# Optimization experiments

Measured on AMD Instinct MI355X. Metric: run time of the kernel, lower is better.

## Reference

```python
import jax, jax.numpy as jnp
import numpy as np
import math

# ---- hyperparameters (from __init__) ----
S = 64.0
M = 0.45
EASY_MARGIN = False
ALPHA = 0.0
BETA = 0.0
EPS_OT = 0.1   # self.eps
NITER = 6      # self.niter
COS_M = math.cos(M)
SIN_M = math.sin(M)
TH = math.cos(math.pi - M)
MM = math.sin(math.pi - M) * M

# ---- shapes ----
B = 24
D_EMB = 512
N_CLASSES = 10000
C_CH = 256   # channels -> number of OT points per image
H = 14       # spatial -> point dim H*H = 196


def setup_inputs() -> dict:
    key = jax.random.key(0)
    k1, k2, k3, k4 = jax.random.split(key, 4)
    embeddings = jax.random.normal(k1, (B, D_EMB), dtype=jnp.float32)
    conv_features = jax.random.normal(k2, (B, C_CH, H, H), dtype=jnp.float32)
    label = jax.random.randint(k3, (B,), 0, 8)
    # nn.init.normal_(kernel, std=0.01)
    kernel = jax.random.normal(k4, (D_EMB, N_CLASSES), dtype=jnp.float32) * 0.01
    return {"embeddings": embeddings, "conv_features": conv_features,
            "kernel": kernel, "label": label, "epoch": 1}


def _cdist(x, y):
    # Euclidean pairwise distance via GEMM: x (n,d), y (m,d) -> (n,m)
    x2 = jnp.sum(x * x, axis=-1)[:, None]
    y2 = jnp.sum(y * y, axis=-1)[None, :]
    d2 = jnp.maximum(x2 + y2 - 2.0 * (x @ y.T), 0.0)
    return jnp.sqrt(d2 + 1e-12)


def _sinkhorn_dist(x, y):
    # Entropic OT distance <T, C> with uniform marginals, log-domain Sinkhorn.
    C = _cdist(x, y)                       # (n, m)
    n, m = C.shape
    log_mu = -jnp.log(jnp.float32(n))
    log_nu = -jnp.log(jnp.float32(m))
    f = jnp.zeros((n,), C.dtype)
    g = jnp.zeros((m,), C.dtype)
    for _ in range(NITER):  # fixed 6 iterations
        f = -EPS_OT * jax.nn.logsumexp((g[None, :] - C) / EPS_OT + log_nu, axis=1)
        g = -EPS_OT * jax.nn.logsumexp((f[:, None] - C) / EPS_OT + log_mu, axis=0)
    T = jnp.exp((f[:, None] + g[None, :] - C) / EPS_OT + log_mu + log_nu)
    return jnp.sum(T * C)


def reference(embeddings, conv_features, kernel, label, epoch):
    b = embeddings.shape[0]
    emb = embeddings / jnp.linalg.norm(embeddings, axis=1, keepdims=True)
    kn = kernel / jnp.linalg.norm(kernel, axis=0, keepdims=True)
    cos_theta = jnp.clip(emb @ kn, -1.0, 1.0)          # (B, n_classes)
    origin_cos = cos_theta

    rows = jnp.arange(b)
    tl = cos_theta[rows, label]                         # target logit (B,)
    sin_t = jnp.sqrt(jnp.maximum(1.0 - tl * tl, 0.0))
    ctm = tl * COS_M - sin_t * SIN_M
    if EASY_MARGIN:
        ftl = jnp.where(tl > 0.0, ctm, tl)
    else:
        ftl = jnp.where(tl > TH, ctm, tl - MM)
    cos_theta = cos_theta.at[rows, label].set(ftl)
    arcfaceloss = cos_theta * S

    # ---- triplet mining on embedding cosine similarities ----
    dists = emb @ emb.T                                 # (B, B) cosine sims
    eq = label[:, None] == label[None, :]               # (B, B) same-class mask
    # diff_low[a,p,n] = cos(a,n) - cos(a,p)
    diff = dists[:, None, :] - dists[:, :, None]        # (a, p, n)
    valid = eq[:, :, None] & (~eq)[:, None, :] & (diff > -ALPHA)
    n_cosine_pair = jnp.sum(valid)

    if epoch >= 0:
        feats = conv_features.reshape(b, conv_features.shape[1], -1)  # (B, C, H*H)
        # batched Sinkhorn distance for all (a,b) image pairs: (B, B)
        D = jax.vmap(lambda xa: jax.vmap(lambda xb: _sinkhorn_dist(xa, xb))(feats))(feats)
        dis = jnp.maximum(D[:, :, None] - D[:, None, :], -BETA)       # (a, p, n)
        hit = valid & (dis > 0.0)
        ot_pair = jnp.sum(hit)
        wass = jnp.sum(jnp.where(hit, dis, 0.0))
        wass_loss = jnp.where(wass > 0.0,
                              wass / jnp.maximum(ot_pair, 1).astype(wass.dtype),
                              jnp.zeros((), wass.dtype))
    else:
        ot_pair = jnp.zeros((), jnp.int32)
        wass_loss = jnp.zeros(())

    return (arcfaceloss, wass_loss, origin_cos * S, n_cosine_pair, ot_pair)
```

## Files before the change

kernel.cpp:

```cpp
#include <hip/hip_runtime.h>
#include <math.h>

#define B_SZ 24
#define D_EMBD 512
#define N_CLS 10000
#define CC 256
#define HH 196

#define NPAIR 276
#define NARC 40
#define NGRAM 36

#define S_SCALE 64.0f
#define COS_M 0.9004471023526769f
#define SIN_M 0.43496553411123023f
#define TH_C (-0.9004471023526769f)
#define MM_C 0.19573449035005357f
#define KSC 14.4269504088896f
#define C2E 0.0693147180559945f

typedef short bfrag8 __attribute__((ext_vector_type(8)));
typedef float facc4 __attribute__((ext_vector_type(4)));

#if __has_builtin(__builtin_amdgcn_exp2f)
#define EXP2F(x) __builtin_amdgcn_exp2f(x)
#else
#define EXP2F(x) exp2f(x)
#endif
#if __has_builtin(__builtin_amdgcn_logf)
#define LOG2F(x) __builtin_amdgcn_logf(x)
#else
#define LOG2F(x) __log2f(x)
#endif

__device__ inline unsigned short f2bf_rne(float x) {
    union { float f; unsigned u; } cv; cv.f = x;
    unsigned r = cv.u + 0x7FFFu + ((cv.u >> 16) & 1u);
    return (unsigned short)(r >> 16);
}
__device__ inline float bf2f(unsigned short h) {
    union { unsigned u; float f; } cv; cv.u = ((unsigned)h) << 16; return cv.f;
}

__global__ __launch_bounds__(1024) void k_fused(const float* __restrict__ emb,
        const float* __restrict__ conv, const float* __restrict__ kern,
        const int* __restrict__ label, float* __restrict__ dists,
        float* __restrict__ Dmat, float* __restrict__ out) {
    const int t = threadIdx.x;
    const int bid = blockIdx.x;

    __shared__ __align__(16) char smem[65536];

    if (bid >= NPAIR) {
        const int sb = bid - NPAIR;
        if (sb >= NARC) {
            const int gid = sb - NARC;
            int l = t & 63, w16 = t >> 6;
            if (gid == 0 && t < B_SZ) Dmat[t * B_SZ + t] = 0.f;
            int pid = gid * 16 + w16;
            if (pid >= B_SZ * B_SZ) return;
            int i = pid / B_SZ, j = pid - (pid / B_SZ) * B_SZ;
            float sij = 0.f, sii = 0.f, sjj = 0.f;
            #pragma unroll
            for (int u = 0; u < 8; ++u) {
                float vi = emb[i*D_EMBD + u*64 + l];
                float vj = emb[j*D_EMBD + u*64 + l];
                sij = fmaf(vi, vj, sij); sii = fmaf(vi, vi, sii); sjj = fmaf(vj, vj, sjj);
            }
            #pragma unroll
            for (int o = 1; o < 64; o <<= 1) {
                sij += __shfl_xor(sij, o, 64);
                sii += __shfl_xor(sii, o, 64);
                sjj += __shfl_xor(sjj, o, 64);
            }
            if (l == 0) dists[pid] = sij * rsqrtf(sii * sjj);
            return;
        }

        float* es = (float*)smem;
        float* inv_s = es + B_SZ * D_EMBD;
        int* lab_s = (int*)(inv_s + B_SZ);

        {
            const float4* s4 = (const float4*)emb;
            float4* d4 = (float4*)es;
            #pragma unroll
            for (int i = 0; i < 3; ++i) d4[i*1024 + t] = s4[i*1024 + t];
        }
        if (t < B_SZ) lab_s[t] = label[t];
        __syncthreads();
        {
            int l = t & 63, w = t >> 6;
            for (int r = w; r < B_SZ; r += 16) {
                float s = 0.f;
                #pragma unroll
                for (int u = 0; u < 8; ++u) { float v = es[r*D_EMBD + u*64 + l]; s = fmaf(v, v, s); }
                #pragma unroll
                for (int o = 1; o < 64; o <<= 1) s += __shfl_xor(s, o, 64);
                if (l == 0) inv_s[r] = rsqrtf(s);
            }
        }
        __syncthreads();

        const int cc = t >> 2, kc = t & 3;
        const int col = sb * 256 + cc;
        const int cL = col < N_CLS ? col : N_CLS - 1;
        float acc[B_SZ];
        #pragma unroll
        for (int r = 0; r < B_SZ; ++r) acc[r] = 0.f;
        float cn = 0.f;
        const int kb0 = kc << 7;
        for (int u = 0; u < 32; ++u) {
            const int um = (u + kc) & 31;
            const int kb = kb0 + (um << 2);
            float kv0 = kern[(kb+0)*N_CLS + cL];
            float kv1 = kern[(kb+1)*N_CLS + cL];
            float kv2 = kern[(kb+2)*N_CLS + cL];
            float kv3 = kern[(kb+3)*N_CLS + cL];
            cn = fmaf(kv0,kv0,cn); cn = fmaf(kv1,kv1,cn);
            cn = fmaf(kv2,kv2,cn); cn = fmaf(kv3,kv3,cn);
            #pragma unroll
            for (int r = 0; r < B_SZ; ++r) {
                const float4 e = *(const float4*)&es[r*D_EMBD + kb];
                acc[r] = fmaf(e.x, kv0, acc[r]);
                acc[r] = fmaf(e.y, kv1, acc[r]);
                acc[r] = fmaf(e.z, kv2, acc[r]);
                acc[r] = fmaf(e.w, kv3, acc[r]);
            }
        }
        cn += __shfl_xor(cn, 1, 64); cn += __shfl_xor(cn, 2, 64);
        #pragma unroll
        for (int r = 0; r < B_SZ; ++r) {
            acc[r] += __shfl_xor(acc[r], 1, 64);
            acc[r] += __shfl_xor(acc[r], 2, 64);
        }
        if (kc == 0 && col < N_CLS) {
            const float invk = rsqrtf(cn);
            #pragma unroll
            for (int r = 0; r < B_SZ; ++r) {
                float cosv = fminf(fmaxf(acc[r] * inv_s[r] * invk, -1.f), 1.f);
                float oc = cosv * S_SCALE;
                float af = oc;
                if (lab_s[r] == col) {
                    float tl = cosv;
                    float sint = sqrtf(fmaxf(1.f - tl*tl, 0.f));
                    float ctm = tl*COS_M - sint*SIN_M;
                    float ftl = (tl > TH_C) ? ctm : (tl - MM_C);
                    af = ftl * S_SCALE;
                }
                out[r*N_CLS + col] = af;
                out[240001 + r*N_CLS + col] = oc;
            }
        }
        return;
    }

    unsigned short* Ah = (unsigned short*)smem;
    unsigned short* Al = Ah + 8192;
    unsigned short* Bh = Al + 8192;
    unsigned short* Bl = Bh + 8192;
    float* rowred = (float*)smem;
    float* colred = rowred + 1024;
    float* rm_l   = colred + 1024;
    float* z_l    = rm_l + 256;
    float* g_l    = z_l + 256;
    float* q_l    = g_l + 256;
    float* p_l    = q_l + 256;
    float* na_s   = p_l + 256;
    float* nb_s   = na_s + 256;
    float* wredF  = nb_s + 256;
    float* wredG  = wredF + 4;
    float* wredD  = wredG + 4;
    float* gsh    = wredD + 16;

    const int w = t >> 6;
    const int wr = w >> 2, wc = w & 3;
    const int q = (t >> 4) & 3, c0 = t & 15;
    const int R0 = wr * 64, C0 = wc * 64;

    int rem = bid, a = 0;
    while (rem >= 23 - a) { rem -= 23 - a; ++a; }
    int b = a + 1 + rem;
    const float* xa = conv + a*CC*HH;
    const float* xb = conv + b*CC*HH;

    const int sn = t >> 2;
    const int sch = t & 3;

    facc4 acc[4][4];
    #pragma unroll
    for (int i = 0; i < 4; ++i)
        #pragma unroll
        for (int j = 0; j < 4; ++j) acc[i][j] = (facc4){0.f, 0.f, 0.f, 0.f};

    float pa = 0.f, pb = 0.f;

    for (int ks = 0; ks < 224; ks += 32) {
        __syncthreads();
        #pragma unroll
        for (int p = 0; p < 2; ++p) {
            int k0 = ks + sch*8;
            const float* src = (p ? xb : xa) + sn*HH + k0;
            float v[8];
            if (k0 + 8 <= HH) {
                const float4* s4 = (const float4*)src;
                float4 u0 = s4[0], u1 = s4[1];
                v[0]=u0.x; v[1]=u0.y; v[2]=u0.z; v[3]=u0.w;
                v[4]=u1.x; v[5]=u1.y; v[6]=u1.z; v[7]=u1.w;
            } else {
                #pragma unroll
                for (int j = 0; j < 8; ++j) v[j] = (k0 + j < HH) ? src[j] : 0.f;
            }
            float ps = 0.f;
            union { unsigned short s[8]; bfrag8 v8; } uh, ul;
            #pragma unroll
            for (int j = 0; j < 8; ++j) {
                ps = fmaf(v[j], v[j], ps);
                unsigned short hb = f2bf_rne(v[j]);
                uh.s[j] = hb;
                ul.s[j] = f2bf_rne(v[j] - bf2f(hb));
            }
            if (p) pb += ps; else pa += ps;
            unsigned short* dh = (p ? Bh : Ah) + sn*32 + sch*8;
            unsigned short* dl = (p ? Bl : Al) + sn*32 + sch*8;
            *(bfrag8*)dh = uh.v8;
            *(bfrag8*)dl = ul.v8;
        }
        __syncthreads();
        bfrag8 bh4[4], bl4[4];
        #pragma unroll
        for (int tj = 0; tj < 4; ++tj) {
            int col = C0 + tj*16 + c0;
            bh4[tj] = *(const bfrag8*)(Bh + col*32 + q*8);
            bl4[tj] = *(const bfrag8*)(Bl + col*32 + q*8);
        }
        #pragma unroll
        for (int ti = 0; ti < 4; ++ti) {
            int row = R0 + ti*16 + c0;
            bfrag8 ah = *(const bfrag8*)(Ah + row*32 + q*8);
            bfrag8 al = *(const bfrag8*)(Al + row*32 + q*8);
            #pragma unroll
            for (int tj = 0; tj < 4; ++tj) {
                acc[ti][tj] = __builtin_amdgcn_mfma_f32_16x16x32_bf16(ah, bh4[tj], acc[ti][tj], 0, 0, 0);
                acc[ti][tj] = __builtin_amdgcn_mfma_f32_16x16x32_bf16(ah, bl4[tj], acc[ti][tj], 0, 0, 0);
                acc[ti][tj] = __builtin_amdgcn_mfma_f32_16x16x32_bf16(al, bh4[tj], acc[ti][tj], 0, 0, 0);
            }
        }
    }
    __syncthreads();

    pa += __shfl_xor(pa, 1, 64); pa += __shfl_xor(pa, 2, 64);
    pb += __shfl_xor(pb, 1, 64); pb += __shfl_xor(pb, 2, 64);
    if (sch == 0) { na_s[sn] = pa; nb_s[sn] = pb; }
    if (t < 256) p_l[t] = 1.f;
    if (t < 4) { wredG[t] = 0.f; wredF[t] = 8.f; }
    if (t == 0) *gsh = 0.f;
    __syncthreads();

    facc4 E[4][4];
    {
        float nbv[4];
        #pragma unroll
        for (int tj = 0; tj < 4; ++tj) nbv[tj] = nb_s[C0 + tj*16 + c0];
        #pragma unroll
        for (int ti = 0; ti < 4; ++ti) {
            facc4 nav = *(const facc4*)&na_s[R0 + ti*16 + q*4];
            #pragma unroll
            for (int tj = 0; tj < 4; ++tj) {
                #pragma unroll
                for (int r = 0; r < 4; ++r) {
                    float d2 = fmaxf(nav[r] + nbv[tj] - 2.f*acc[ti][tj][r], 0.f);
                    E[ti][tj][r] = KSC * sqrtf(d2 + 1e-12f);
                }
            }
        }
    }

    const int istar = ((c0&1)<<3) | ((c0&2)<<1) | ((c0&4)>>1) | ((c0&8)>>3);
    const int rowstar = R0 + (istar>>2)*16 + q*4 + (istar&3);
    const int tjstar = ((q&1)<<1) | (q>>1);
    const int colstar = C0 + tjstar*16 + c0;

    {
        float v16[16];
        #pragma unroll
        for (int ti = 0; ti < 4; ++ti)
            #pragma unroll
            for (int r = 0; r < 4; ++r)
                v16[ti*4+r] = fminf(fminf(E[ti][0][r], E[ti][1][r]),
                                    fminf(E[ti][2][r], E[ti][3][r]));
        #pragma unroll
        for (int p = 0; p < 4; ++p) {
            const int m = 1 << p, hsz = 8 >> p;
            const bool hi = (c0 >> p) & 1;
            #pragma unroll
            for (int j = 0; j < hsz; ++j) {
                float mine = hi ? v16[j+hsz] : v16[j];
                float send = hi ? v16[j] : v16[j+hsz];
                v16[j] = fminf(mine, __shfl_xor(send, m, 64));
            }
        }
        rowred[wc*256 + rowstar] = v16[0];
    }
    __syncthreads();
    if (t < 256)
        rm_l[t] = fminf(fminf(rowred[t], rowred[256+t]), fminf(rowred[512+t], rowred[768+t]));
    __syncthreads();

    #pragma unroll
    for (int ti = 0; ti < 4; ++ti) {
        facc4 rmv = *(const facc4*)&rm_l[R0 + ti*16 + q*4];
        #pragma unroll
        for (int tj = 0; tj < 4; ++tj)
            #pragma unroll
            for (int r = 0; r < 4; ++r)
                E[ti][tj][r] = EXP2F(rmv[r] - E[ti][tj][r]);
    }

    #pragma unroll 1
    for (int it = 0; it < 6; ++it) {
        float Gstale = fmaxf(fmaxf(wredG[0], wredG[1]), fmaxf(wredG[2], wredG[3]));
        float MS     = fmaxf(fmaxf(wredF[0], wredF[1]), fmaxf(wredF[2], wredF[3]));
        float P4[4];
        #pragma unroll
        for (int tj = 0; tj < 4; ++tj) P4[tj] = p_l[C0 + tj*16 + c0];
        float v16[16];
        #pragma unroll
        for (int ti = 0; ti < 4; ++ti)
            #pragma unroll
            for (int r = 0; r < 4; ++r) {
                float s = 0.f;
                #pragma unroll
                for (int tj = 0; tj < 4; ++tj) s = fmaf(E[ti][tj][r], P4[tj], s);
                v16[ti*4+r] = s;
            }
        #pragma unroll
        for (int p = 0; p < 4; ++p) {
            const int m = 1 << p, hsz = 8 >> p;
            const bool hi = (c0 >> p) & 1;
            #pragma unroll
            for (int j = 0; j < hsz; ++j) {
                float mine = hi ? v16[j+hsz] : v16[j];
                float send = hi ? v16[j] : v16[j+hsz];
                v16[j] = mine + __shfl_xor(send, m, 64);
            }
        }
        rowred[wc*256 + rowstar] = v16[0];
        __syncthreads();
        if (t < 256) {
            float GS = *gsh;
            float s = rowred[t] + rowred[256+t] + rowred[512+t] + rowred[768+t];
            float z = 8.f - GS - LOG2F(s);
            z_l[t] = z;
            q_l[t] = EXP2F(z - MS);
            float m = z;
            #pragma unroll
            for (int o = 1; o < 64; o <<= 1) m = fmaxf(m, __shfl_xor(m, o, 64));
            if ((t & 63) == 0) wredF[t >> 6] = m;
        }
        __syncthreads();
        float Q[16];
        #pragma unroll
        for (int ti = 0; ti < 4; ++ti) {
            facc4 qv = *(const facc4*)&q_l[R0 + ti*16 + q*4];
            #pragma unroll
            for (int r = 0; r < 4; ++r) Q[ti*4+r] = qv[r];
        }
        float w4[4];
        #pragma unroll
        for (int tj = 0; tj < 4; ++tj) {
            float s = 0.f;
            #pragma unroll
            for (int ti = 0; ti < 4; ++ti)
                #pragma unroll
                for (int r = 0; r < 4; ++r) s = fmaf(E[ti][tj][r], Q[ti*4+r], s);
            w4[tj] = s;
        }
        #pragma unroll
        for (int p = 0; p < 2; ++p) {
            const int m = 16 << p, hsz = 2 >> p;
            const bool hi = (q >> p) & 1;
            #pragma unroll
            for (int j = 0; j < hsz; ++j) {
                float mine = hi ? w4[j+hsz] : w4[j];
                float send = hi ? w4[j] : w4[j+hsz];
                w4[j] = mine + __shfl_xor(send, m, 64);
            }
        }
        colred[wr*256 + colstar] = w4[0];
        __syncthreads();
        if (t < 256) {
            float s = colred[t] + colred[256+t] + colred[512+t] + colred[768+t];
            float G = 8.f - MS - LOG2F(s);
            g_l[t] = G;
            p_l[t] = EXP2F(G - Gstale);
            float m = G;
            #pragma unroll
            for (int o = 1; o < 64; o <<= 1) m = fmaxf(m, __shfl_xor(m, o, 64));
            if ((t & 63) == 0) wredG[t >> 6] = m;
            if (t == 0) *gsh = Gstale;
        }
        __syncthreads();
    }

    {
        float G4[4];
        #pragma unroll
        for (int tj = 0; tj < 4; ++tj) G4[tj] = g_l[C0 + tj*16 + c0] - 16.f;
        float d = 0.f;
        #pragma unroll
        for (int ti = 0; ti < 4; ++ti) {
            facc4 zv = *(const facc4*)&z_l[R0 + ti*16 + q*4];
            facc4 rmv = *(const facc4*)&rm_l[R0 + ti*16 + q*4];
            #pragma unroll
            for (int tj = 0; tj < 4; ++tj) {
                #pragma unroll
                for (int r = 0; r < 4; ++r) {
                    float e = fmaxf(E[ti][tj][r], 1e-45f);
                    float lE = LOG2F(e);
                    float ce = rmv[r] - lE;
                    d = fmaf(EXP2F(zv[r] + G4[tj] + lE), ce, d);
                }
            }
        }
        d *= C2E;
        #pragma unroll
        for (int o = 1; o < 64; o <<= 1) d += __shfl_xor(d, o, 64);
        if ((t & 63) == 0) wredD[w] = d;
        __syncthreads();
        if (t == 0) {
            float s = 0.f;
            #pragma unroll
            for (int i = 0; i < 16; ++i) s += wredD[i];
            Dmat[a*B_SZ + b] = s;
            Dmat[b*B_SZ + a] = s;
        }
    }
}

__global__ __launch_bounds__(256) void k_fin(const int* __restrict__ label,
        const float* __restrict__ dists, const float* __restrict__ Dmat,
        float* __restrict__ out) {
    const int t = threadIdx.x;
    __shared__ float ds[576], Dm[576];
    __shared__ int lab[B_SZ];
    __shared__ float wls[4]; __shared__ int wnp[4], wot[4];
    for (int i = t; i < 576; i += 256) { ds[i] = dists[i]; Dm[i] = Dmat[i]; }
    if (t < B_SZ) lab[t] = label[t];
    __syncthreads();
    int np = 0, ot = 0; float wsum = 0.f;
    for (int idx = t; idx < 24*24*24; idx += 256) {
        int a2 = idx / 576;
        int rest = idx - a2*576;
        int p2 = rest / 24;
        int n2 = rest - p2*24;
        int la = lab[a2];
        if (la == lab[p2] && la != lab[n2]) {
            float diff = ds[a2*24 + n2] - ds[a2*24 + p2];
            if (diff > 0.f) {
                ++np;
                float dd = Dm[a2*24 + p2] - Dm[a2*24 + n2];
                if (dd > 0.f) { ++ot; wsum += dd; }
            }
        }
    }
    #pragma unroll
    for (int o = 1; o < 64; o <<= 1) {
        np += __shfl_xor(np, o, 64);
        ot += __shfl_xor(ot, o, 64);
        wsum += __shfl_xor(wsum, o, 64);
    }
    int w = t >> 6;
    if ((t & 63) == 0) { wnp[w] = np; wot[w] = ot; wls[w] = wsum; }
    __syncthreads();
    if (t == 0) {
        int tnp = wnp[0]+wnp[1]+wnp[2]+wnp[3];
        int tot = wot[0]+wot[1]+wot[2]+wot[3];
        float tws = wls[0]+wls[1]+wls[2]+wls[3];
        int den = tot > 1 ? tot : 1;
        float wl = (tws > 0.f) ? tws / (float)den : 0.f;
        out[240000] = wl;
        out[480001] = (float)tnp;
        out[480002] = (float)tot;
    }
}

extern "C" void kernel_launch(void* const* d_in, const int* in_sizes, int n_in,
                              void* d_out, int out_size, void* d_ws, size_t ws_size,
                              hipStream_t stream) {
    (void)in_sizes; (void)n_in; (void)out_size; (void)ws_size;
    const float* emb  = (const float*)d_in[0];
    const float* conv = (const float*)d_in[1];
    const float* kern = (const float*)d_in[2];
    const int*   lab  = (const int*)d_in[3];
    float* out = (float*)d_out;
    float* ws  = (float*)d_ws;
    float* dists = ws;
    float* Dmat  = ws + 576;

    k_fused<<<NPAIR + NARC + NGRAM, 1024, 0, stream>>>(emb, conv, kern, lab, dists, Dmat, out);
    k_fin<<<1, 256, 0, stream>>>(lab, dists, Dmat, out);
}
```

Before: 193.7 us.

## Precompute bf16 hi/lo split and row norms of conv features in a prepass kernel

Adds a prepass kernel that converts each image's conv features once into padded bf16 hi/lo planes plus squared row norms. The fused pair kernel then streams these preconverted planes through double-buffered shared memory into the MFMA GEMM, so the fp32-to-bf16 split is not redone for every one of the 276 image pairs. The old per-pair conversion path is kept as a fallback for when the workspace is too small. The cost is an extra kernel launch, extra global traffic for the bf16 planes, and doubled static shared memory, which may limit occupancy.

```diff
diff --git a/kernel.cpp b/kernel.cpp
--- a/kernel.cpp
+++ b/kernel.cpp
@@ -6,6 +6,7 @@
 #define N_CLS 10000
 #define CC 256
 #define HH 196
+#define KPAD 224
 
 #define NPAIR 276
 #define NARC 40
@@ -42,14 +43,52 @@
     union { unsigned u; float f; } cv; cv.u = ((unsigned)h) << 16; return cv.f;
 }
 
-__global__ __launch_bounds__(1024) void k_fused(const float* __restrict__ emb,
-        const float* __restrict__ conv, const float* __restrict__ kern,
-        const int* __restrict__ label, float* __restrict__ dists,
+__global__ __launch_bounds__(1024) void k_pre(const float* __restrict__ conv,
+        unsigned short* __restrict__ hiP, unsigned short* __restrict__ loP,
+        float* __restrict__ nrm) {
+    const int t = threadIdx.x;
+    const int img = blockIdx.x;
+    const int row = t >> 2, sch = t & 3;
+    const float* src = conv + (img*CC + row)*HH;
+    unsigned short* hb = hiP + (img*CC + row)*KPAD;
+    unsigned short* lb = loP + (img*CC + row)*KPAD;
+    float ps = 0.f;
+    for (int c = sch; c < 28; c += 4) {
+        const int k0 = c*8;
+        float v[8];
+        if (k0 + 8 <= HH) {
+            const float4* s4 = (const float4*)(src + k0);
+            float4 u0 = s4[0], u1 = s4[1];
+            v[0]=u0.x; v[1]=u0.y; v[2]=u0.z; v[3]=u0.w;
+            v[4]=u1.x; v[5]=u1.y; v[6]=u1.z; v[7]=u1.w;
+        } else {
+            #pragma unroll
+            for (int j = 0; j < 8; ++j) v[j] = (k0 + j < HH) ? src[k0 + j] : 0.f;
+        }
+        union { unsigned short s[8]; bfrag8 v8; } uh, ul;
+        #pragma unroll
+        for (int j = 0; j < 8; ++j) {
+            ps = fmaf(v[j], v[j], ps);
+            unsigned short hbv = f2bf_rne(v[j]);
+            uh.s[j] = hbv;
+            ul.s[j] = f2bf_rne(v[j] - bf2f(hbv));
+        }
+        *(bfrag8*)(hb + k0) = uh.v8;
+        *(bfrag8*)(lb + k0) = ul.v8;
+    }
+    ps += __shfl_xor(ps, 1, 64); ps += __shfl_xor(ps, 2, 64);
+    if (sch == 0) nrm[img*CC + row] = ps;
+}
+
+__global__ __launch_bounds__(1024) void k_fused_pre(const float* __restrict__ emb,
+        const float* __restrict__ kern, const int* __restrict__ label,
+        const unsigned short* __restrict__ hiP, const unsigned short* __restrict__ loP,
+        const float* __restrict__ nrm, float* __restrict__ dists,
         float* __restrict__ Dmat, float* __restrict__ out) {
     const int t = threadIdx.x;
     const int bid = blockIdx.x;
 
-    __shared__ __align__(16) char smem[65536];
+    __shared__ __align__(16) char smem[131072];
 
     if (bid >= NPAIR) {
         const int sb = bid - NPAIR;
@@ -80,7 +119,399 @@
         float* es = (float*)smem;
         float* inv_s = es + B_SZ * D_EMBD;
         int* lab_s = (int*)(inv_s + B_SZ);
-
+        {
+            const float4* s4 = (const float4*)emb;
+            float4* d4 = (float4*)es;
+            #pragma unroll
+            for (int i = 0; i < 3; ++i) d4[i*1024 + t] = s4[i*1024 + t];
+        }
+        if (t < B_SZ) lab_s[t] = label[t];
+        __syncthreads();
+        {
+            int l = t & 63, w = t >> 6;
+            for (int r = w; r < B_SZ; r += 16) {
+                float s = 0.f;
+                #pragma unroll
+                for (int u = 0; u < 8; ++u) { float v = es[r*D_EMBD + u*64 + l]; s = fmaf(v, v, s); }
+                #pragma unroll
+                for (int o = 1; o < 64; o <<= 1) s += __shfl_xor(s, o, 64);
+                if (l == 0) inv_s[r] = rsqrtf(s);
+            }
+        }
+        __syncthreads();
+
+        const int cc = t >> 2, kc = t & 3;
+        const int col = sb * 256 + cc;
+        const int cL = col < N_CLS ? col : N_CLS - 1;
+        float acc[B_SZ];
+        #pragma unroll
+        for (int r = 0; r < B_SZ; ++r) acc[r] = 0.f;
+        float cn = 0.f;
+        const int kb0 = kc << 7;
+        for (int u = 0; u < 32; ++u) {
+            const int um = (u + kc) & 31;
+            const int kb = kb0 + (um << 2);
+            float kv0 = kern[(kb+0)*N_CLS + cL];
+            float kv1 = kern[(kb+1)*N_CLS + cL];
+            float kv2 = kern[(kb+2)*N_CLS + cL];
+            float kv3 = kern[(kb+3)*N_CLS + cL];
+            cn = fmaf(kv0,kv0,cn); cn = fmaf(kv1,kv1,cn);
+            cn = fmaf(kv2,kv2,cn); cn = fmaf(kv3,kv3,cn);
+            #pragma unroll
+            for (int r = 0; r < B_SZ; ++r) {
+                const float4 e = *(const float4*)&es[r*D_EMBD + kb];
+                acc[r] = fmaf(e.x, kv0, acc[r]);
+                acc[r] = fmaf(e.y, kv1, acc[r]);
+                acc[r] = fmaf(e.z, kv2, acc[r]);
+                acc[r] = fmaf(e.w, kv3, acc[r]);
+            }
+        }
+        cn += __shfl_xor(cn, 1, 64); cn += __shfl_xor(cn, 2, 64);
+        #pragma unroll
+        for (int r = 0; r < B_SZ; ++r) {
+            acc[r] += __shfl_xor(acc[r], 1, 64);
+            acc[r] += __shfl_xor(acc[r], 2, 64);
+        }
+        if (kc == 0 && col < N_CLS) {
+            const float invk = rsqrtf(cn);
+            #pragma unroll
+            for (int r = 0; r < B_SZ; ++r) {
+                float cosv = fminf(fmaxf(acc[r] * inv_s[r] * invk, -1.f), 1.f);
+                float oc = cosv * S_SCALE;
+                float af = oc;
+                if (lab_s[r] == col) {
+                    float tl = cosv;
+                    float sint = sqrtf(fmaxf(1.f - tl*tl, 0.f));
+                    float ctm = tl*COS_M - sint*SIN_M;
+                    float ftl = (tl > TH_C) ? ctm : (tl - MM_C);
+                    af = ftl * S_SCALE;
+                }
+                out[r*N_CLS + col] = af;
+                out[240001 + r*N_CLS + col] = oc;
+            }
+        }
+        return;
+    }
+
+    unsigned short* SB = (unsigned short*)smem;
+    float* rowred = (float*)smem;
+    float* colred = rowred + 1024;
+    float* rm_l   = colred + 1024;
+    float* z_l    = rm_l + 256;
+    float* g_l    = z_l + 256;
+    float* q_l    = g_l + 256;
+    float* p_l    = q_l + 256;
+    float* na_s   = p_l + 256;
+    float* nb_s   = na_s + 256;
+    float* wredF  = nb_s + 256;
+    float* wredG  = wredF + 4;
+    float* wredD  = wredG + 4;
+    float* gsh    = wredD + 16;
+
+    const int w = t >> 6;
+    const int wr = w >> 2, wc = w & 3;
+    const int q = (t >> 4) & 3, c0 = t & 15;
+    const int R0 = wr * 64, C0 = wc * 64;
+
+    int rem = bid, a = 0;
+    while (rem >= 23 - a) { rem -= 23 - a; ++a; }
+    int b = a + 1 + rem;
+
+    const int sn = t >> 2;
+    const int sch = t & 3;
+    const unsigned short* gAh = hiP + (a*CC + sn)*KPAD + sch*8;
+    const unsigned short* gAl = loP + (a*CC + sn)*KPAD + sch*8;
+    const unsigned short* gBh = hiP + (b*CC + sn)*KPAD + sch*8;
+    const unsigned short* gBl = loP + (b*CC + sn)*KPAD + sch*8;
+    const int so = sn*32 + sch*8;
+
+    facc4 acc[4][4];
+    #pragma unroll
+    for (int i = 0; i < 4; ++i)
+        #pragma unroll
+        for (int j = 0; j < 4; ++j) acc[i][j] = (facc4){0.f, 0.f, 0.f, 0.f};
+
+    uint4 pAh, pAl, pBh, pBl;
+    pAh = *(const uint4*)(gAh); pAl = *(const uint4*)(gAl);
+    pBh = *(const uint4*)(gBh); pBl = *(const uint4*)(gBl);
+    {
+        unsigned short* base = SB;
+        *(uint4*)(base + so)          = pAh;
+        *(uint4*)(base + 8192 + so)   = pAl;
+        *(uint4*)(base + 16384 + so)  = pBh;
+        *(uint4*)(base + 24576 + so)  = pBl;
+    }
+    pAh = *(const uint4*)(gAh + 32); pAl = *(const uint4*)(gAl + 32);
+    pBh = *(const uint4*)(gBh + 32); pBl = *(const uint4*)(gBl + 32);
+
+    for (int s = 0; s < 7; ++s) {
+        __syncthreads();
+        if (s < 6) {
+            unsigned short* base = SB + ((s + 1) & 1) * 32768;
+            *(uint4*)(base + so)          = pAh;
+            *(uint4*)(base + 8192 + so)   = pAl;
+            *(uint4*)(base + 16384 + so)  = pBh;
+            *(uint4*)(base + 24576 + so)  = pBl;
+        }
+        unsigned short* Ah = SB + (s & 1) * 32768;
+        unsigned short* Al = Ah + 8192;
+        unsigned short* Bh = Al + 8192;
+        unsigned short* Bl = Bh + 8192;
+        bfrag8 bh4[4], bl4[4];
+        #pragma unroll
+        for (int tj = 0; tj < 4; ++tj) {
+            int col = C0 + tj*16 + c0;
+            bh4[tj] = *(const bfrag8*)(Bh + col*32 + q*8);
+            bl4[tj] = *(const bfrag8*)(Bl + col*32 + q*8);
+        }
+        #pragma unroll
+        for (int ti = 0; ti < 4; ++ti) {
+            int row = R0 + ti*16 + c0;
+            bfrag8 ah = *(const bfrag8*)(Ah + row*32 + q*8);
+            bfrag8 al = *(const bfrag8*)(Al + row*32 + q*8);
+            #pragma unroll
+            for (int tj = 0; tj < 4; ++tj) {
+                acc[ti][tj] = __builtin_amdgcn_mfma_f32_16x16x32_bf16(ah, bh4[tj], acc[ti][tj], 0, 0, 0);
+                acc[ti][tj] = __builtin_amdgcn_mfma_f32_16x16x32_bf16(ah, bl4[tj], acc[ti][tj], 0, 0, 0);
+                acc[ti][tj] = __builtin_amdgcn_mfma_f32_16x16x32_bf16(al, bh4[tj], acc[ti][tj], 0, 0, 0);
+            }
+        }
+        if (s < 5) {
+            const int ko = (s + 2) * 32;
+            pAh = *(const uint4*)(gAh + ko); pAl = *(const uint4*)(gAl + ko);
+            pBh = *(const uint4*)(gBh + ko); pBl = *(const uint4*)(gBl + ko);
+        }
+    }
+    __syncthreads();
+
+    if (t < 256) {
+        na_s[t] = nrm[a*CC + t];
+        nb_s[t] = nrm[b*CC + t];
+        p_l[t] = 1.f;
+    }
+    if (t < 4) { wredG[t] = 0.f; wredF[t] = 8.f; }
+    if (t == 0) *gsh = 0.f;
+    __syncthreads();
+
+    facc4 E[4][4];
+    {
+        float nbv[4];
+        #pragma unroll
+        for (int tj = 0; tj < 4; ++tj) nbv[tj] = nb_s[C0 + tj*16 + c0];
+        #pragma unroll
+        for (int ti = 0; ti < 4; ++ti) {
+            facc4 nav = *(const facc4*)&na_s[R0 + ti*16 + q*4];
+            #pragma unroll
+            for (int tj = 0; tj < 4; ++tj) {
+                #pragma unroll
+                for (int r = 0; r < 4; ++r) {
+                    float d2 = fmaxf(nav[r] + nbv[tj] - 2.f*acc[ti][tj][r], 0.f);
+                    E[ti][tj][r] = KSC * sqrtf(d2 + 1e-12f);
+                }
+            }
+        }
+    }
+
+    const int istar = ((c0&1)<<3) | ((c0&2)<<1) | ((c0&4)>>1) | ((c0&8)>>3);
+    const int rowstar = R0 + (istar>>2)*16 + q*4 + (istar&3);
+    const int tjstar = ((q&1)<<1) | (q>>1);
+    const int colstar = C0 + tjstar*16 + c0;
+
+    {
+        float v16[16];
+        #pragma unroll
+        for (int ti = 0; ti < 4; ++ti)
+            #pragma unroll
+            for (int r = 0; r < 4; ++r)
+                v16[ti*4+r] = fminf(fminf(E[ti][0][r], E[ti][1][r]),
+                                    fminf(E[ti][2][r], E[ti][3][r]));
+        #pragma unroll
+        for (int p = 0; p < 4; ++p) {
+            const int m = 1 << p, hsz = 8 >> p;
+            const bool hi = (c0 >> p) & 1;
+            #pragma unroll
+            for (int j = 0; j < hsz; ++j) {
+                float mine = hi ? v16[j+hsz] : v16[j];
+                float send = hi ? v16[j] : v16[j+hsz];
+                v16[j] = fminf(mine, __shfl_xor(send, m, 64));
+            }
+        }
+        rowred[wc*256 + rowstar] = v16[0];
+    }
+    __syncthreads();
+    if (t < 256)
+        rm_l[t] = fminf(fminf(rowred[t], rowred[256+t]), fminf(rowred[512+t], rowred[768+t]));
+    __syncthreads();
+
+    #pragma unroll
+    for (int ti = 0; ti < 4; ++ti) {
+        facc4 rmv = *(const facc4*)&rm_l[R0 + ti*16 + q*4];
+        #pragma unroll
+        for (int tj = 0; tj < 4; ++tj)
+            #pragma unroll
+            for (int r = 0; r < 4; ++r)
+                E[ti][tj][r] = EXP2F(rmv[r] - E[ti][tj][r]);
+    }
+
+    #pragma unroll 1
+    for (int it = 0; it < 6; ++it) {
+        float Gstale = fmaxf(fmaxf(wredG[0], wredG[1]), fmaxf(wredG[2], wredG[3]));
+        float MS     = fmaxf(fmaxf(wredF[0], wredF[1]), fmaxf(wredF[2], wredF[3]));
+        float P4[4];
+        #pragma unroll
+        for (int tj = 0; tj < 4; ++tj) P4[tj] = p_l[C0 + tj*16 + c0];
+        float v16[16];
+        #pragma unroll
+        for (int ti = 0; ti < 4; ++ti)
+            #pragma unroll
+            for (int r = 0; r < 4; ++r) {
+                float s = 0.f;
+                #pragma unroll
+                for (int tj = 0; tj < 4; ++tj) s = fmaf(E[ti][tj][r], P4[tj], s);
+                v16[ti*4+r] = s;
+            }
+        #pragma unroll
+        for (int p = 0; p < 4; ++p) {
+            const int m = 1 << p, hsz = 8 >> p;
+            const bool hi = (c0 >> p) & 1;
+            #pragma unroll
+            for (int j = 0; j < hsz; ++j) {
+                float mine = hi ? v16[j+hsz] : v16[j];
+                float send = hi ? v16[j] : v16[j+hsz];
+                v16[j] = mine + __shfl_xor(send, m, 64);
+            }
+        }
+        rowred[wc*256 + rowstar] = v16[0];
+        __syncthreads();
+        if (t < 256) {
+            float GS = *gsh;
+            float s = rowred[t] + rowred[256+t] + rowred[512+t] + rowred[768+t];
+            float z = 8.f - GS - LOG2F(s);
+            z_l[t] = z;
+            q_l[t] = EXP2F(z - MS);
+            float m = z;
+            #pragma unroll
+            for (int o = 1; o < 64; o <<= 1) m = fmaxf(m, __shfl_xor(m, o, 64));
+            if ((t & 63) == 0) wredF[t >> 6] = m;
+        }
+        __syncthreads();
+        float Q[16];
+        #pragma unroll
+        for (int ti = 0; ti < 4; ++ti) {
+            facc4 qv = *(const facc4*)&q_l[R0 + ti*16 + q*4];
+            #pragma unroll
+            for (int r = 0; r < 4; ++r) Q[ti*4+r] = qv[r];
+        }
+        float w4[4];
+        #pragma unroll
+        for (int tj = 0; tj < 4; ++tj) {
+            float s = 0.f;
+            #pragma unroll
+            for (int ti = 0; ti < 4; ++ti)
+                #pragma unroll
+                for (int r = 0; r < 4; ++r) s = fmaf(E[ti][tj][r], Q[ti*4+r], s);
+            w4[tj] = s;
+        }
+        #pragma unroll
+        for (int p = 0; p < 2; ++p) {
+            const int m = 16 << p, hsz = 2 >> p;
+            const bool hi = (q >> p) & 1;
+            #pragma unroll
+            for (int j = 0; j < hsz; ++j) {
+                float mine = hi ? w4[j+hsz] : w4[j];
+                float send = hi ? w4[j] : w4[j+hsz];
+                w4[j] = mine + __shfl_xor(send, m, 64);
+            }
+        }
+        colred[wr*256 + colstar] = w4[0];
+        __syncthreads();
+        if (t < 256) {
+            float s = colred[t] + colred[256+t] + colred[512+t] + colred[768+t];
+            float G = 8.f - MS - LOG2F(s);
+            g_l[t] = G;
+            p_l[t] = EXP2F(G - Gstale);
+            float m = G;
+            #pragma unroll
+            for (int o = 1; o < 64; o <<= 1) m = fmaxf(m, __shfl_xor(m, o, 64));
+            if ((t & 63) == 0) wredG[t >> 6] = m;
+            if (t == 0) *gsh = Gstale;
+        }
+        __syncthreads();
+    }
+
+    {
+        float G4[4];
+        #pragma unroll
+        for (int tj = 0; tj < 4; ++tj) G4[tj] = g_l[C0 + tj*16 + c0] - 16.f;
+        float d = 0.f;
+        #pragma unroll
+        for (int ti = 0; ti < 4; ++ti) {
+            facc4 zv = *(const facc4*)&z_l[R0 + ti*16 + q*4];
+            facc4 rmv = *(const facc4*)&rm_l[R0 + ti*16 + q*4];
+            #pragma unroll
+            for (int tj = 0; tj < 4; ++tj) {
+                #pragma unroll
+                for (int r = 0; r < 4; ++r) {
+                    float e = fmaxf(E[ti][tj][r], 1e-45f);
+                    float lE = LOG2F(e);
+                    float ce = rmv[r] - lE;
+                    d = fmaf(EXP2F(zv[r] + G4[tj] + lE), ce, d);
+                }
+            }
+        }
+        d *= C2E;
+        #pragma unroll
+        for (int o = 1; o < 64; o <<= 1) d += __shfl_xor(d, o, 64);
+        if ((t & 63) == 0) wredD[w] = d;
+        __syncthreads();
+        if (t == 0) {
+            float s = 0.f;
+            #pragma unroll
+            for (int i = 0; i < 16; ++i) s += wredD[i];
+            Dmat[a*B_SZ + b] = s;
+            Dmat[b*B_SZ + a] = s;
+        }
+    }
+}
+
+__global__ __launch_bounds__(1024) void k_fused_loc(const float* __restrict__ emb,
+        const float* __restrict__ conv, const float* __restrict__ kern,
+        const int* __restrict__ label, float* __restrict__ dists,
+        float* __restrict__ Dmat, float* __restrict__ out) {
+    const int t = threadIdx.x;
+    const int bid = blockIdx.x;
+
+    __shared__ __align__(16) char smem[65536];
+
+    if (bid >= NPAIR) {
+        const int sb = bid - NPAIR;
+        if (sb >= NARC) {
+            const int gid = sb - NARC;
+            int l = t & 63, w16 = t >> 6;
+            if (gid == 0 && t < B_SZ) Dmat[t * B_SZ + t] = 0.f;
+            int pid = gid * 16 + w16;
+            if (pid >= B_SZ * B_SZ) return;
+            int i = pid / B_SZ, j = pid - (pid / B_SZ) * B_SZ;
+            float sij = 0.f, sii = 0.f, sjj = 0.f;
+            #pragma unroll
+            for (int u = 0; u < 8; ++u) {
+                float vi = emb[i*D_EMBD + u*64 + l];
+                float vj = emb[j*D_EMBD + u*64 + l];
+                sij = fmaf(vi, vj, sij); sii = fmaf(vi, vi, sii); sjj = fmaf(vj, vj, sjj);
+            }
+            #pragma unroll
+            for (int o = 1; o < 64; o <<= 1) {
+                sij += __shfl_xor(sij, o, 64);
+                sii += __shfl_xor(sii, o, 64);
+                sjj += __shfl_xor(sjj, o, 64);
+            }
+            if (l == 0) dists[pid] = sij * rsqrtf(sii * sjj);
+            return;
+        }
+
+        float* es = (float*)smem;
+        float* inv_s = es + B_SZ * D_EMBD;
+        int* lab_s = (int*)(inv_s + B_SZ);
         {
             const float4* s4 = (const float4*)emb;
             float4* d4 = (float4*)es;
@@ -488,7 +919,7 @@
 extern "C" void kernel_launch(void* const* d_in, const int* in_sizes, int n_in,
                               void* d_out, int out_size, void* d_ws, size_t ws_size,
                               hipStream_t stream) {
-    (void)in_sizes; (void)n_in; (void)out_size; (void)ws_size;
+    (void)in_sizes; (void)n_in; (void)out_size;
     const float* emb  = (const float*)d_in[0];
     const float* conv = (const float*)d_in[1];
     const float* kern = (const float*)d_in[2];
@@ -498,6 +929,18 @@
     float* dists = ws;
     float* Dmat  = ws + 576;
 
-    k_fused<<<NPAIR + NARC + NGRAM, 1024, 0, stream>>>(emb, conv, kern, lab, dists, Dmat, out);
+    const size_t NEED = 7296u * 4u + 2u * (size_t)(24 * CC * KPAD) * 2u;
+
+    if (ws_size >= NEED) {
+        float* nrm = ws + 1152;
+        unsigned short* hiP = (unsigned short*)(ws + 7296);
+        unsigned short* loP = hiP + 24*CC*KPAD;
+        k_pre<<<24, 1024, 0, stream>>>(conv, hiP, loP, nrm);
+        k_fused_pre<<<NPAIR + NARC + NGRAM, 1024, 0, stream>>>(emb, kern, lab, hiP, loP, nrm,
+                                                               dists, Dmat, out);
+    } else {
+        k_fused_loc<<<NPAIR + NARC + NGRAM, 1024, 0, stream>>>(emb, conv, kern, lab,
+                                                               dists, Dmat, out);
+    }
     k_fin<<<1, 256, 0, stream>>>(lab, dists, Dmat, out);
 }
```

Result: no change. 191.4 us (-1.2%).
